# Optimization experiments

Measured on AMD Instinct MI355X. Metric: run time of the kernel, lower is better.

The kernel has to match this reference:

```python
import jax, jax.numpy as jnp
import numpy as np

# Config constants (match init_kwargs)
E = 16          # n_routed_experts
G = 4           # n_groups
TOPK_G = 2      # topk_groups
K = 4           # n_activated_experts
ROUTE_SCALE = 2.5446


def setup_inputs() -> dict:
    key = jax.random.key(0)
    ks = jax.random.split(key, 9)
    T, D, H = 2048, 1024, 704
    HS = 2 * H  # shared FFN hidden = n_shared_experts * expert_hidden_dim
    sc = lambda k, shape, fan_in: (jax.random.normal(k, shape, jnp.float32)
                                   * (fan_in ** -0.5))
    return {
        "x":      jax.random.normal(ks[0], (T, D), jnp.float32),
        "gate_w": sc(ks[1], (E, D), D),
        "gate_b": jnp.zeros((E,), jnp.float32),       # V3 routing bias (init 0)
        "w1":     sc(ks[2], (E, H, D), D),            # gate proj per expert
        "w3":     sc(ks[3], (E, H, D), D),            # up proj per expert
        "w2":     sc(ks[4], (E, D, H), H),            # down proj per expert
        "ws1":    sc(ks[5], (HS, D), D),              # shared FFN gate proj
        "ws3":    sc(ks[6], (HS, D), D),              # shared FFN up proj
        "ws2":    sc(ks[7], (D, HS), HS),             # shared FFN down proj
    }


def _gate(x, gate_w, gate_b):
    """DeepSeek-V3 sigmoid gate with bias routing + group-limited masking."""
    T = x.shape[0]
    logits = x @ gate_w.T                                   # [T, E]
    scores = jax.nn.sigmoid(logits).astype(jnp.float32)     # original_scores
    routing = scores + gate_b                               # bias only affects routing
    g = routing.reshape(T, G, E // G)
    # use_bias=True -> group score = sum of top-2 routing scores in group
    group_scores = jnp.sum(jax.lax.top_k(g, 2)[0], axis=-1)     # [T, G]
    top_groups = jax.lax.top_k(group_scores, TOPK_G)[1]         # [T, TOPK_G]
    keep = jnp.any(jnp.arange(G)[None, :, None] == top_groups[:, None, :],
                   axis=-1)                                     # [T, G]
    routing = jnp.where(keep[:, :, None], g, -jnp.inf).reshape(T, E)
    idx = jax.lax.top_k(routing, K)[1]                          # [T, K]
    w = jnp.take_along_axis(scores, idx, axis=1)                # un-biased weights
    w = w / jnp.clip(jnp.sum(w, axis=-1, keepdims=True), 1e-9)  # sigmoid renorm
    w = (w * ROUTE_SCALE).astype(x.dtype)
    return w, idx


def reference(x, gate_w, gate_b, w1, w3, w2, ws1, ws3, ws2):
    T, D = x.shape
    weights, idx = _gate(x, gate_w, gate_b)                 # [T,K], [T,K]
    # Dense dispatch/combine matrix: combine[t, e] = gate weight (0 if unrouted)
    combine = jnp.zeros((T, E), x.dtype).at[
        jnp.arange(T)[:, None], idx].add(weights)           # [T, E]
    # Routed experts: SwiGLU per expert, grouped GEMMs
    hg = jnp.einsum('td,ehd->eth', x, w1)                   # [E, T, H]
    hu = jnp.einsum('td,ehd->eth', x, w3)                   # [E, T, H]
    eo = jnp.einsum('eth,edh->etd', jax.nn.silu(hg) * hu, w2)  # [E, T, D]
    y_routed = jnp.einsum('etd,te->td', eo, combine)        # [T, D]
    # Shared experts (always active SwiGLU)
    y_shared = (jax.nn.silu(x @ ws1.T) * (x @ ws3.T)) @ ws2.T
    return y_routed + y_shared
```

## Files before the change

### kernel.cpp

```cpp
#include <hip/hip_runtime.h>
#include <hip/hip_bf16.h>
#include <math.h>

typedef __attribute__((ext_vector_type(4))) float   f32x4;
typedef __attribute__((ext_vector_type(8))) short   short8;
typedef __attribute__((ext_vector_type(8))) __bf16  bf16x8;

union SB8 { short8 s; bf16x8 b; };

__device__ __forceinline__ short f2bf(float f) {
  union { float f; unsigned u; } v; v.f = f;
  unsigned r = v.u + 0x7fffu + ((v.u >> 16) & 1u);
  return (short)(r >> 16);
}

__device__ __forceinline__ short8 cvt8(f32x4 a, f32x4 b) {
  short8 r;
  r[0] = f2bf(a[0]); r[1] = f2bf(a[1]); r[2] = f2bf(a[2]); r[3] = f2bf(a[3]);
  r[4] = f2bf(b[0]); r[5] = f2bf(b[1]); r[6] = f2bf(b[2]); r[7] = f2bf(b[3]);
  return r;
}

__device__ __forceinline__ void ldsload16(const short* g, short* l) {
  __builtin_amdgcn_global_load_lds(
      (const __attribute__((address_space(1))) unsigned int*)g,
      (__attribute__((address_space(3))) unsigned int*)l, 16, 0, 0);
}

#define TT   2048
#define DD   1024
#define HH   704
#define HSS  1408
#define EE   16
#define CAP  2048
#define CSTR 32

#define O1  2097152ULL
#define O2  13631488ULL
#define O3  25165824ULL
#define O4  36700160ULL
#define O5  38141952ULL
#define O6  39583744ULL
#define CVT_TOTAL 41025536ULL

#define W2SZ    11534336ULL
#define WS1SZ   1441792ULL
#define WS1END  26607616ULL
#define CVTA_TOTAL  28049408ULL
#define CVTA_BLOCKS 3424
#define GATE_BLOCKS 512

__global__ __launch_bounds__(256)
void gate_cvt(const float* __restrict__ x,  const float* __restrict__ w1,
              const float* __restrict__ w3, const float* __restrict__ s1,
              const float* __restrict__ s3, short* __restrict__ dst,
              const float* __restrict__ gw, const float* __restrict__ gb,
              int* __restrict__ counts, int* __restrict__ tok,
              float* __restrict__ wgt, int* __restrict__ eslot)
{
  if (blockIdx.x >= GATE_BLOCKS) {
    const int tid = threadIdx.x;
    const size_t base = (size_t)(blockIdx.x - GATE_BLOCKS) * 8192;
    const float* sp[4]; short* dp[4];
    #pragma unroll
    for (int k = 0; k < 4; k++) {
      const size_t sb = base + (size_t)k * 2048;
      const float* src; size_t doff;
      if      (sb < O1)     { src = x  + sb;            doff = sb; }
      else if (sb < O2)     { src = w1 + (sb - O1);     doff = sb; }
      else if (sb < O3)     { src = w3 + (sb - O2);     doff = sb; }
      else if (sb < WS1END) { src = s1 + (sb - O3);     doff = sb + W2SZ; }
      else                  { src = s3 + (sb - WS1END); doff = sb + W2SZ; }
      sp[k] = src + tid * 8;
      dp[k] = dst + doff + tid * 8;
    }
    f32x4 va[8];
    #pragma unroll
    for (int k = 0; k < 4; k++) {
      va[2 * k]     = *(const f32x4*)(sp[k]);
      va[2 * k + 1] = *(const f32x4*)(sp[k] + 4);
    }
    #pragma unroll
    for (int k = 0; k < 4; k++)
      *(short8*)(dp[k]) = cvt8(va[2 * k], va[2 * k + 1]);
    return;
  }

  const int lane = threadIdx.x & 63;
  const int wid  = threadIdx.x >> 6;
  const int t    = blockIdx.x * 4 + wid;
  const int e    = lane & 15;
  const int p    = lane >> 4;

  const float* xp = x + (size_t)t * DD + p * 256;
  const float* gp = gw + (size_t)e * DD + p * 256;

  double a0 = 0.0, a1 = 0.0, a2 = 0.0, a3 = 0.0;
  #pragma unroll 8
  for (int i = 0; i < 64; i++) {
    f32x4 xa = *(const f32x4*)(xp + i * 4);
    f32x4 ga = *(const f32x4*)(gp + i * 4);
    a0 += (double)xa[0] * (double)ga[0];
    a1 += (double)xa[1] * (double)ga[1];
    a2 += (double)xa[2] * (double)ga[2];
    a3 += (double)xa[3] * (double)ga[3];
  }
  double acc = (a0 + a1) + (a2 + a3);
  acc += __shfl_xor(acc, 16);
  acc += __shfl_xor(acc, 32);
  float accf = (float)acc;

  float lf[EE], sc[EE], r[EE];
  #pragma unroll
  for (int j = 0; j < EE; j++) lf[j] = __shfl(accf, j);
  #pragma unroll
  for (int j = 0; j < EE; j++) {
    sc[j] = 1.f / (1.f + expf(-lf[j]));
    r[j] = sc[j] + gb[j];
  }
  float gs[4];
  #pragma unroll
  for (int g = 0; g < 4; g++) {
    float m1 = -1e30f, m2 = -1e30f;
    #pragma unroll
    for (int j = 0; j < 4; j++) {
      float v = r[g * 4 + j];
      if (v > m1) { m2 = m1; m1 = v; }
      else if (v > m2) { m2 = v; }
    }
    gs[g] = m1 + m2;
  }
  int g1 = 0, g2 = -1; float b1 = -1e30f, b2 = -1e30f;
  #pragma unroll
  for (int g = 0; g < 4; g++) {
    if (gs[g] > b1) { b2 = b1; g2 = g1; b1 = gs[g]; g1 = g; }
    else if (gs[g] > b2) { b2 = gs[g]; g2 = g; }
  }
  int idx[4]; float wv[4]; float wsum = 0.f;
  unsigned used = 0;
  #pragma unroll
  for (int k = 0; k < 4; k++) {
    float best = -1e30f; int bi = 0;
    #pragma unroll
    for (int j = 0; j < EE; j++) {
      int g = j >> 2;
      bool keep = (g == g1) || (g == g2);
      if (keep && !((used >> j) & 1) && r[j] > best) { best = r[j]; bi = j; }
    }
    used |= 1u << bi; idx[k] = bi; wv[k] = sc[bi]; wsum += sc[bi];
  }
  float div = wsum < 1e-9f ? 1e-9f : wsum;
  if (lane < 4) {
    float w = wv[lane] / div * 2.5446f;
    int slot = atomicAdd(&counts[idx[lane] * CSTR], 1);
    tok[idx[lane] * CAP + slot] = t;
    wgt[idx[lane] * CAP + slot] = w;
    eslot[t * 4 + lane] = (idx[lane] << 16) | slot;
  }
}

#define WAIT_PREV_TILE()  do { \
    asm volatile("s_waitcnt vmcnt(4)" ::: "memory"); \
    __builtin_amdgcn_sched_barrier(0); \
    __builtin_amdgcn_s_barrier(); \
    __builtin_amdgcn_sched_barrier(0); } while (0)
#define WAIT_LAST_TILE()  do { \
    asm volatile("s_waitcnt vmcnt(0)" ::: "memory"); \
    __builtin_amdgcn_sched_barrier(0); \
    __builtin_amdgcn_s_barrier(); \
    __builtin_amdgcn_sched_barrier(0); } while (0)
#define END_TILE_BARRIER() do { \
    __builtin_amdgcn_sched_barrier(0); \
    __builtin_amdgcn_s_barrier(); } while (0)

__global__ __launch_bounds__(512, 2)
void gemm1_merged(const short* __restrict__ xb, const short* __restrict__ w1b,
                  const short* __restrict__ w3b, const short* __restrict__ ws1b,
                  const short* __restrict__ ws3b, short* __restrict__ act_r,
                  short* __restrict__ act_s, const int* __restrict__ counts,
                  const int* __restrict__ tok,
                  const float* __restrict__ w2f, const float* __restrict__ ws2f,
                  short* __restrict__ w2bd, short* __restrict__ ws2bd)
{
  const int F = blockIdx.x + 11 * (blockIdx.y + 16 * blockIdx.z);
  const int r8 = F & 7, rank = F >> 3;
  int z, Mt, Ntc;
  if (rank < 22) {
    z = 0;
    const int p = rank * 8 + r8;
    Mt = p / 11; Ntc = p - Mt * 11;
  } else if (rank < 374) {
    const int rr = rank - 22;
    z = 1 + r8 + 8 * (rr / 176);
    const int p = rr % 176;
    Mt = p / 11; Ntc = p - Mt * 11;
  } else {
    z = 17;
    const int p = (rank - 374) * 8 + r8;
    Mt = p / 22; Ntc = p - Mt * 22;
  }

  if (z == 0) {
    const int bid = Mt * 11 + Ntc;
    const int tid = threadIdx.x;
    for (int s = 0; s < 3; s++) {
      const size_t base = (size_t)bid * 73728 + (size_t)s * 24576;
      const float* sp[6]; short* dp[6];
      #pragma unroll
      for (int k = 0; k < 6; k++) {
        const size_t sb = base + (size_t)k * 4096;
        if (sb < W2SZ) {
          sp[k] = w2f + sb + tid * 8;
          dp[k] = w2bd + sb + tid * 8;
        } else {
          const size_t o = sb - W2SZ;
          sp[k] = ws2f + o + tid * 8;
          dp[k] = ws2bd + o + tid * 8;
        }
      }
      f32x4 va[12];
      #pragma unroll
      for (int k = 0; k < 6; k++) {
        va[2 * k]     = *(const f32x4*)(sp[k]);
        va[2 * k + 1] = *(const f32x4*)(sp[k] + 4);
      }
      #pragma unroll
      for (int k = 0; k < 6; k++)
        *(short8*)(dp[k]) = cvt8(va[2 * k], va[2 * k + 1]);
    }
    return;
  }

  const bool routed = (z <= EE);
  const int e = z - 1;

  int cnt, N, rowbase = 0;
  const short *W1, *W3;
  short* act;
  if (routed) {
    cnt = counts[e * CSTR];
    if (Mt * 128 >= cnt) return;
    int rb = 0;
    for (int i = 0; i < e; i++) rb += counts[i * CSTR];
    rowbase = rb;
    N = HH;
    W1 = w1b + (size_t)e * HH * DD;
    W3 = w3b + (size_t)e * HH * DD;
    act = act_r;
  } else {
    cnt = TT; N = HSS; W1 = ws1b; W3 = ws3b; act = act_s;
  }
  const int NtB = Ntc * 64;

  __shared__ __align__(16) short lA [2][128 * 64];
  __shared__ __align__(16) short lB1[2][64 * 64];
  __shared__ __align__(16) short lB3[2][64 * 64];

  const int tid = threadIdx.x, lane = tid & 63, wv = tid >> 6;
  const int srow = lane >> 3, schunk = lane & 7, scg = schunk ^ srow;

  const short* pa[2]; const short* pb1; const short* pb3;
  #pragma unroll
  for (int i = 0; i < 2; i++) {
    const int g = wv * 2 + i;
    int arow = Mt * 128 + g * 8 + srow;
    if (routed) {
      int slot = arow < cnt ? arow : cnt - 1;
      arow = tok[e * CAP + slot];
    }
    pa[i] = xb + (size_t)arow * DD + scg * 8;
  }
  {
    const int brow = NtB + wv * 8 + srow;
    pb1 = W1 + (size_t)brow * DD + scg * 8;
    pb3 = W3 + (size_t)brow * DD + scg * 8;
  }

  f32x4 acc1[4], acc3[4];
  #pragma unroll
  for (int i = 0; i < 4; i++) { acc1[i] = (f32x4)0.f; acc3[i] = (f32x4)0.f; }

  const int q = lane >> 4, r7 = lane & 7, hi = (lane & 15) >> 3;
  const int wc = wv & 3, mh = wv >> 2;

#define STAGE1(c, kk) do { \
    ldsload16(pa[0] + (kk), &lA [c][(wv * 2 + 0) * 512]); \
    ldsload16(pa[1] + (kk), &lA [c][(wv * 2 + 1) * 512]); \
    ldsload16(pb1  + (kk),  &lB1[c][wv * 512]); \
    ldsload16(pb3  + (kk),  &lB3[c][wv * 512]); } while (0)

#define GEMM1_BODY(c) do { \
    _Pragma("unroll") for (int kc = 0; kc < 2; kc++) { \
      const int cx = (kc * 4 + q) ^ r7; \
      SB8 b1f, b3f; \
      b1f.s = *(const short8*)(&lB1[c][((wc * 2 + hi) * 64 + r7 * 8 + cx) * 8]); \
      b3f.s = *(const short8*)(&lB3[c][((wc * 2 + hi) * 64 + r7 * 8 + cx) * 8]); \
      _Pragma("unroll") for (int mt = 0; mt < 4; mt++) { \
        SB8 af; af.s = *(const short8*)(&lA[c][((2 * (mh * 4 + mt) + hi) * 64 + r7 * 8 + cx) * 8]); \
        acc1[mt] = __builtin_amdgcn_mfma_f32_16x16x32_bf16(af.b, b1f.b, acc1[mt], 0, 0, 0); \
        acc3[mt] = __builtin_amdgcn_mfma_f32_16x16x32_bf16(af.b, b3f.b, acc3[mt], 0, 0, 0); \
      } } } while (0)

  STAGE1(0, 0);
  int cur = 0;
  for (int kk = 64; kk < DD; kk += 64) {
    STAGE1(cur ^ 1, kk);
    WAIT_PREV_TILE();
    GEMM1_BODY(cur);
    END_TILE_BARRIER();
    cur ^= 1;
  }
  WAIT_LAST_TILE();
  GEMM1_BODY(cur);

  const int quad = lane >> 4, lcol = lane & 15;
  const int col = NtB + wc * 16 + lcol;
  #pragma unroll
  for (int mt = 0; mt < 4; mt++) {
    #pragma unroll
    for (int rg = 0; rg < 4; rg++) {
      const int r = Mt * 128 + (mh * 4 + mt) * 16 + quad * 4 + rg;
      if (r < cnt) {
        float g = acc1[mt][rg], u = acc3[mt][rg];
        float a = g / (1.f + __expf(-g)) * u;
        act[(size_t)(rowbase + r) * N + col] = f2bf(a);
      }
    }
  }
#undef STAGE1
#undef GEMM1_BODY
}

__global__ __launch_bounds__(512, 2)
void gemm2_merged(const short* __restrict__ act_r, const short* __restrict__ act_s,
                  const short* __restrict__ w2b, const short* __restrict__ ws2b,
                  float* __restrict__ y, float* __restrict__ outr,
                  const int* __restrict__ counts, const float* __restrict__ wgt)
{
  const int F = blockIdx.x + 8 * (blockIdx.y + 16 * blockIdx.z);
  const int r8 = F & 7, rank = F >> 3;
  int z, Mt, Nt;
  if (rank < 256) {
    z = r8 + 8 * (rank >> 7);
    const int p = rank & 127;
    Mt = p >> 3; Nt = p & 7;
  } else {
    z = 16;
    const int p = (rank - 256) * 8 + r8;
    Mt = p >> 3; Nt = p & 7;
  }

  const bool routed = (z < EE);

  int cnt, Kd, rowbase = 0;
  const short *A, *W;
  if (routed) {
    cnt = counts[z * CSTR];
    if (Mt * 128 >= cnt) return;
    int rb = 0;
    for (int i = 0; i < z; i++) rb += counts[i * CSTR];
    rowbase = rb;
    Kd = HH;
    A = act_r + (size_t)rowbase * HH;
    W = w2b + (size_t)z * DD * HH;
  } else {
    cnt = TT; Kd = HSS; A = act_s; W = ws2b;
  }

  __shared__ __align__(16) short lA[2][128 * 64];
  __shared__ __align__(16) short lB[2][128 * 64];

  const int tid = threadIdx.x, lane = tid & 63, wv = tid >> 6;
  const int srow = lane >> 3, schunk = lane & 7, scg = schunk ^ srow;

  const short* pa[2]; const short* pb[2];
  #pragma unroll
  for (int i = 0; i < 2; i++) {
    const int g = wv * 2 + i;
    int arow = Mt * 128 + g * 8 + srow;
    if (arow >= cnt) arow = cnt - 1;
    pa[i] = A + (size_t)arow * Kd + scg * 8;
    const int brow = Nt * 128 + g * 8 + srow;
    pb[i] = W + (size_t)brow * Kd + scg * 8;
  }

  f32x4 acc[4][2];
  #pragma unroll
  for (int i = 0; i < 4; i++) { acc[i][0] = (f32x4)0.f; acc[i][1] = (f32x4)0.f; }

  const int q = lane >> 4, r7 = lane & 7, hi = (lane & 15) >> 3;
  const int wc = wv & 3, mh = wv >> 2;

#define STAGE2(c, kk) do { \
    ldsload16(pa[0] + (kk), &lA[c][(wv * 2 + 0) * 512]); \
    ldsload16(pa[1] + (kk), &lA[c][(wv * 2 + 1) * 512]); \
    ldsload16(pb[0] + (kk), &lB[c][(wv * 2 + 0) * 512]); \
    ldsload16(pb[1] + (kk), &lB[c][(wv * 2 + 1) * 512]); } while (0)

#define GEMM2_BODY(c) do { \
    _Pragma("unroll") for (int kc = 0; kc < 2; kc++) { \
      const int cx = (kc * 4 + q) ^ r7; \
      SB8 bf[2]; \
      _Pragma("unroll") for (int ntl = 0; ntl < 2; ntl++) { \
        const int a16 = ((wc * 2 + ntl) * 2 + hi) * 64 + r7 * 8 + cx; \
        bf[ntl].s = *(const short8*)(&lB[c][a16 * 8]); \
      } \
      _Pragma("unroll") for (int mt = 0; mt < 4; mt++) { \
        const int a16 = (2 * (mh * 4 + mt) + hi) * 64 + r7 * 8 + cx; \
        SB8 af; af.s = *(const short8*)(&lA[c][a16 * 8]); \
        acc[mt][0] = __builtin_amdgcn_mfma_f32_16x16x32_bf16(af.b, bf[0].b, acc[mt][0], 0, 0, 0); \
        acc[mt][1] = __builtin_amdgcn_mfma_f32_16x16x32_bf16(af.b, bf[1].b, acc[mt][1], 0, 0, 0); \
      } } } while (0)

  STAGE2(0, 0);
  int cur = 0;
  for (int kk = 64; kk < Kd; kk += 64) {
    STAGE2(cur ^ 1, kk);
    WAIT_PREV_TILE();
    GEMM2_BODY(cur);
    END_TILE_BARRIER();
    cur ^= 1;
  }
  WAIT_LAST_TILE();
  GEMM2_BODY(cur);

  const int quad = lane >> 4, lcol = lane & 15;
  #pragma unroll
  for (int mt = 0; mt < 4; mt++) {
    #pragma unroll
    for (int ntl = 0; ntl < 2; ntl++) {
      const int col = Nt * 128 + (wc * 2 + ntl) * 16 + lcol;
      #pragma unroll
      for (int rg = 0; rg < 4; rg++) {
        const int slot = Mt * 128 + (mh * 4 + mt) * 16 + quad * 4 + rg;
        const float v = acc[mt][ntl][rg];
        if (routed) {
          if (slot < cnt) {
            const float w = wgt[z * CAP + slot];
            outr[(size_t)(rowbase + slot) * DD + col] = w * v;
          }
        } else {
          y[(size_t)slot * DD + col] = v;
        }
      }
    }
  }
#undef STAGE2
#undef GEMM2_BODY
}

__global__ __launch_bounds__(256)
void combine_kernel(float* __restrict__ y, const float* __restrict__ outr,
                    const int* __restrict__ eslot, const int* __restrict__ counts)
{
  const int t = blockIdx.x;
  const int d = threadIdx.x * 4;

  int offs[EE];
  int s = 0;
  #pragma unroll
  for (int i = 0; i < EE; i++) { offs[i] = s; s += counts[i * CSTR]; }

  f32x4 accv = *(f32x4*)(y + (size_t)t * DD + d);
  #pragma unroll
  for (int k = 0; k < 4; k++) {
    const int es = eslot[t * 4 + k];
    const int row = offs[es >> 16] + (es & 0xFFFF);
    accv += *(const f32x4*)(outr + (size_t)row * DD + d);
  }
  *(f32x4*)(y + (size_t)t * DD + d) = accv;
}

extern "C" void kernel_launch(void* const* d_in, const int* in_sizes, int n_in,
                              void* d_out, int out_size, void* d_ws, size_t ws_size,
                              hipStream_t stream) {
  const float* x      = (const float*)d_in[0];
  const float* gate_w = (const float*)d_in[1];
  const float* gate_b = (const float*)d_in[2];
  const float* w1     = (const float*)d_in[3];
  const float* w3     = (const float*)d_in[4];
  const float* w2     = (const float*)d_in[5];
  const float* ws1    = (const float*)d_in[6];
  const float* ws3    = (const float*)d_in[7];
  const float* ws2    = (const float*)d_in[8];
  float* y = (float*)d_out;

  char* ws = (char*)d_ws;
  int*   counts = (int*)ws;
  int*   tok    = (int*)(ws + 2048);
  float* wgt    = (float*)(ws + 2048 + (size_t)EE * CAP * 4);
  int*   eslot  = (int*)(ws + 2048 + (size_t)EE * CAP * 8);
  short* bf     = (short*)(ws + 2048 + (size_t)EE * CAP * 8 + (size_t)TT * 16);
  short* xb   = bf;
  short* w1b  = bf + O1;
  short* w3b  = bf + O2;
  short* w2b  = bf + O3;
  short* ws1b = bf + O4;
  short* ws3b = bf + O5;
  short* ws2b = bf + O6;
  short* act_r = bf + CVT_TOTAL;
  short* act_s = act_r + (size_t)8192 * HH;
  float* outr = (float*)(bf + O1);

  (void)hipMemsetAsync(counts, 0, EE * CSTR * sizeof(int), stream);

  gate_cvt<<<GATE_BLOCKS + CVTA_BLOCKS, 256, 0, stream>>>(
      x, w1, w3, ws1, ws3, bf,
      gate_w, gate_b, counts, tok, wgt, eslot);

  gemm1_merged<<<dim3(11, TT / 128, EE + 3), 512, 0, stream>>>(
      xb, w1b, w3b, ws1b, ws3b, act_r, act_s, counts, tok,
      w2, ws2, w2b, ws2b);

  gemm2_merged<<<dim3(DD / 128, TT / 128, EE + 1), 512, 0, stream>>>(
      act_r, act_s, w2b, ws2b, y, outr, counts, wgt);

  combine_kernel<<<TT, 256, 0, stream>>>(y, outr, eslot, counts);
}
```

Measured before the change: 300.6 us.

## Convert weights to bf16 inside GEMM staging instead of separate pre-pass

```diff
diff --git a/kernel.cpp b/kernel.cpp
--- a/kernel.cpp
+++ b/kernel.cpp
@@ -34,26 +34,12 @@
 #define EE   16
 #define CAP  2048
 #define CSTR 32
-
-#define O1  2097152ULL
-#define O2  13631488ULL
-#define O3  25165824ULL
-#define O4  36700160ULL
-#define O5  38141952ULL
-#define O6  39583744ULL
-#define CVT_TOTAL 41025536ULL
-
-#define W2SZ    11534336ULL
-#define WS1SZ   1441792ULL
-#define WS1END  26607616ULL
-#define CVTA_TOTAL  28049408ULL
-#define CVTA_BLOCKS 3424
+#define XSZ  2097152ULL
 #define GATE_BLOCKS 512
+#define XCVT_BLOCKS 256
 
 __global__ __launch_bounds__(256)
-void gate_cvt(const float* __restrict__ x,  const float* __restrict__ w1,
-              const float* __restrict__ w3, const float* __restrict__ s1,
-              const float* __restrict__ s3, short* __restrict__ dst,
+void gate_cvt(const float* __restrict__ x, short* __restrict__ xb,
               const float* __restrict__ gw, const float* __restrict__ gb,
               int* __restrict__ counts, int* __restrict__ tok,
               float* __restrict__ wgt, int* __restrict__ eslot)
@@ -61,28 +47,15 @@
   if (blockIdx.x >= GATE_BLOCKS) {
     const int tid = threadIdx.x;
     const size_t base = (size_t)(blockIdx.x - GATE_BLOCKS) * 8192;
-    const float* sp[4]; short* dp[4];
+    f32x4 va[8];
     #pragma unroll
     for (int k = 0; k < 4; k++) {
-      const size_t sb = base + (size_t)k * 2048;
-      const float* src; size_t doff;
-      if      (sb < O1)     { src = x  + sb;            doff = sb; }
-      else if (sb < O2)     { src = w1 + (sb - O1);     doff = sb; }
-      else if (sb < O3)     { src = w3 + (sb - O2);     doff = sb; }
-      else if (sb < WS1END) { src = s1 + (sb - O3);     doff = sb + W2SZ; }
-      else                  { src = s3 + (sb - WS1END); doff = sb + W2SZ; }
-      sp[k] = src + tid * 8;
-      dp[k] = dst + doff + tid * 8;
-    }
-    f32x4 va[8];
-    #pragma unroll
-    for (int k = 0; k < 4; k++) {
-      va[2 * k]     = *(const f32x4*)(sp[k]);
-      va[2 * k + 1] = *(const f32x4*)(sp[k] + 4);
+      va[2 * k]     = *(const f32x4*)(x + base + (size_t)k * 2048 + tid * 8);
+      va[2 * k + 1] = *(const f32x4*)(x + base + (size_t)k * 2048 + tid * 8 + 4);
     }
     #pragma unroll
     for (int k = 0; k < 4; k++)
-      *(short8*)(dp[k]) = cvt8(va[2 * k], va[2 * k + 1]);
+      *(short8*)(xb + base + (size_t)k * 2048 + tid * 8) = cvt8(va[2 * k], va[2 * k + 1]);
     return;
   }
 
@@ -159,96 +132,53 @@
   }
 }
 
-#define WAIT_PREV_TILE()  do { \
-    asm volatile("s_waitcnt vmcnt(4)" ::: "memory"); \
-    __builtin_amdgcn_sched_barrier(0); \
-    __builtin_amdgcn_s_barrier(); \
-    __builtin_amdgcn_sched_barrier(0); } while (0)
-#define WAIT_LAST_TILE()  do { \
+#define PIPE_VM_WAIT() do { \
     asm volatile("s_waitcnt vmcnt(0)" ::: "memory"); \
     __builtin_amdgcn_sched_barrier(0); \
     __builtin_amdgcn_s_barrier(); \
     __builtin_amdgcn_sched_barrier(0); } while (0)
-#define END_TILE_BARRIER() do { \
+#define PIPE_LGKM_BAR() do { \
+    asm volatile("s_waitcnt lgkmcnt(0)" ::: "memory"); \
     __builtin_amdgcn_sched_barrier(0); \
-    __builtin_amdgcn_s_barrier(); } while (0)
+    __builtin_amdgcn_s_barrier(); \
+    __builtin_amdgcn_sched_barrier(0); } while (0)
 
 __global__ __launch_bounds__(512, 2)
-void gemm1_merged(const short* __restrict__ xb, const short* __restrict__ w1b,
-                  const short* __restrict__ w3b, const short* __restrict__ ws1b,
-                  const short* __restrict__ ws3b, short* __restrict__ act_r,
-                  short* __restrict__ act_s, const int* __restrict__ counts,
-                  const int* __restrict__ tok,
-                  const float* __restrict__ w2f, const float* __restrict__ ws2f,
-                  short* __restrict__ w2bd, short* __restrict__ ws2bd)
+void gemm1_merged(const short* __restrict__ xb,
+                  const float* __restrict__ w1f, const float* __restrict__ w3f,
+                  const float* __restrict__ ws1f, const float* __restrict__ ws3f,
+                  short* __restrict__ act_r, short* __restrict__ act_s,
+                  const int* __restrict__ counts, const int* __restrict__ tok)
 {
   const int F = blockIdx.x + 11 * (blockIdx.y + 16 * blockIdx.z);
   const int r8 = F & 7, rank = F >> 3;
   int z, Mt, Ntc;
-  if (rank < 22) {
-    z = 0;
-    const int p = rank * 8 + r8;
-    Mt = p / 11; Ntc = p - Mt * 11;
-  } else if (rank < 374) {
-    const int rr = rank - 22;
-    z = 1 + r8 + 8 * (rr / 176);
-    const int p = rr % 176;
-    Mt = p / 11; Ntc = p - Mt * 11;
+  if (rank < 352) {
+    z = r8 + 8 * (rank / 176);
+    const int p = rank % 176;
+    Mt = p / 11; Ntc = p % 11;
   } else {
-    z = 17;
-    const int p = (rank - 374) * 8 + r8;
-    Mt = p / 22; Ntc = p - Mt * 22;
-  }
-
-  if (z == 0) {
-    const int bid = Mt * 11 + Ntc;
-    const int tid = threadIdx.x;
-    for (int s = 0; s < 3; s++) {
-      const size_t base = (size_t)bid * 73728 + (size_t)s * 24576;
-      const float* sp[6]; short* dp[6];
-      #pragma unroll
-      for (int k = 0; k < 6; k++) {
-        const size_t sb = base + (size_t)k * 4096;
-        if (sb < W2SZ) {
-          sp[k] = w2f + sb + tid * 8;
-          dp[k] = w2bd + sb + tid * 8;
-        } else {
-          const size_t o = sb - W2SZ;
-          sp[k] = ws2f + o + tid * 8;
-          dp[k] = ws2bd + o + tid * 8;
-        }
-      }
-      f32x4 va[12];
-      #pragma unroll
-      for (int k = 0; k < 6; k++) {
-        va[2 * k]     = *(const f32x4*)(sp[k]);
-        va[2 * k + 1] = *(const f32x4*)(sp[k] + 4);
-      }
-      #pragma unroll
-      for (int k = 0; k < 6; k++)
-        *(short8*)(dp[k]) = cvt8(va[2 * k], va[2 * k + 1]);
-    }
-    return;
-  }
-
-  const bool routed = (z <= EE);
-  const int e = z - 1;
-
+    z = 16;
+    const int p = (rank - 352) * 8 + r8;
+    Mt = p / 22; Ntc = p % 22;
+  }
+
+  const bool routed = (z < EE);
   int cnt, N, rowbase = 0;
-  const short *W1, *W3;
+  const float *W1, *W3;
   short* act;
   if (routed) {
-    cnt = counts[e * CSTR];
+    cnt = counts[z * CSTR];
     if (Mt * 128 >= cnt) return;
     int rb = 0;
-    for (int i = 0; i < e; i++) rb += counts[i * CSTR];
+    for (int i = 0; i < z; i++) rb += counts[i * CSTR];
     rowbase = rb;
     N = HH;
-    W1 = w1b + (size_t)e * HH * DD;
-    W3 = w3b + (size_t)e * HH * DD;
+    W1 = w1f + (size_t)z * HH * DD;
+    W3 = w3f + (size_t)z * HH * DD;
     act = act_r;
   } else {
-    cnt = TT; N = HSS; W1 = ws1b; W3 = ws3b; act = act_s;
+    cnt = TT; N = HSS; W1 = ws1f; W3 = ws3f; act = act_s;
   }
   const int NtB = Ntc * 64;
 
@@ -259,35 +189,44 @@
   const int tid = threadIdx.x, lane = tid & 63, wv = tid >> 6;
   const int srow = lane >> 3, schunk = lane & 7, scg = schunk ^ srow;
 
-  const short* pa[2]; const short* pb1; const short* pb3;
+  const short* pa[2];
   #pragma unroll
   for (int i = 0; i < 2; i++) {
     const int g = wv * 2 + i;
     int arow = Mt * 128 + g * 8 + srow;
     if (routed) {
       int slot = arow < cnt ? arow : cnt - 1;
-      arow = tok[e * CAP + slot];
+      arow = tok[z * CAP + slot];
     }
     pa[i] = xb + (size_t)arow * DD + scg * 8;
   }
+  const float *pb1f, *pb3f;
   {
     const int brow = NtB + wv * 8 + srow;
-    pb1 = W1 + (size_t)brow * DD + scg * 8;
-    pb3 = W3 + (size_t)brow * DD + scg * 8;
+    pb1f = W1 + (size_t)brow * DD + scg * 8;
+    pb3f = W3 + (size_t)brow * DD + scg * 8;
   }
 
   f32x4 acc1[4], acc3[4];
   #pragma unroll
   for (int i = 0; i < 4; i++) { acc1[i] = (f32x4)0.f; acc3[i] = (f32x4)0.f; }
+  f32x4 rb1[2], rb3[2];
 
   const int q = lane >> 4, r7 = lane & 7, hi = (lane & 15) >> 3;
   const int wc = wv & 3, mh = wv >> 2;
-
-#define STAGE1(c, kk) do { \
-    ldsload16(pa[0] + (kk), &lA [c][(wv * 2 + 0) * 512]); \
-    ldsload16(pa[1] + (kk), &lA [c][(wv * 2 + 1) * 512]); \
-    ldsload16(pb1  + (kk),  &lB1[c][wv * 512]); \
-    ldsload16(pb3  + (kk),  &lB3[c][wv * 512]); } while (0)
+  const int wofs = wv * 512 + srow * 64 + schunk * 8;
+
+#define STAGE1_ISSUE(c, kk) do { \
+    ldsload16(pa[0] + (kk), &lA[c][(wv * 2 + 0) * 512]); \
+    ldsload16(pa[1] + (kk), &lA[c][(wv * 2 + 1) * 512]); \
+    rb1[0] = *(const f32x4*)(pb1f + (kk)); \
+    rb1[1] = *(const f32x4*)(pb1f + (kk) + 4); \
+    rb3[0] = *(const f32x4*)(pb3f + (kk)); \
+    rb3[1] = *(const f32x4*)(pb3f + (kk) + 4); } while (0)
+
+#define STAGE1_WRITE(c) do { \
+    *(short8*)(&lB1[c][wofs]) = cvt8(rb1[0], rb1[1]); \
+    *(short8*)(&lB3[c][wofs]) = cvt8(rb3[0], rb3[1]); } while (0)
 
 #define GEMM1_BODY(c) do { \
     _Pragma("unroll") for (int kc = 0; kc < 2; kc++) { \
@@ -301,16 +240,20 @@
         acc3[mt] = __builtin_amdgcn_mfma_f32_16x16x32_bf16(af.b, b3f.b, acc3[mt], 0, 0, 0); \
       } } } while (0)
 
-  STAGE1(0, 0);
+  STAGE1_ISSUE(0, 0);
+  asm volatile("s_waitcnt vmcnt(0)" ::: "memory");
+  __builtin_amdgcn_sched_barrier(0);
+  STAGE1_WRITE(0);
+  PIPE_LGKM_BAR();
   int cur = 0;
   for (int kk = 64; kk < DD; kk += 64) {
-    STAGE1(cur ^ 1, kk);
-    WAIT_PREV_TILE();
+    STAGE1_ISSUE(cur ^ 1, kk);
     GEMM1_BODY(cur);
-    END_TILE_BARRIER();
+    PIPE_VM_WAIT();
+    STAGE1_WRITE(cur ^ 1);
+    PIPE_LGKM_BAR();
     cur ^= 1;
   }
-  WAIT_LAST_TILE();
   GEMM1_BODY(cur);
 
   const int quad = lane >> 4, lcol = lane & 15;
@@ -327,13 +270,14 @@
       }
     }
   }
-#undef STAGE1
+#undef STAGE1_ISSUE
+#undef STAGE1_WRITE
 #undef GEMM1_BODY
 }
 
 __global__ __launch_bounds__(512, 2)
 void gemm2_merged(const short* __restrict__ act_r, const short* __restrict__ act_s,
-                  const short* __restrict__ w2b, const short* __restrict__ ws2b,
+                  const float* __restrict__ w2f, const float* __restrict__ ws2f,
                   float* __restrict__ y, float* __restrict__ outr,
                   const int* __restrict__ counts, const float* __restrict__ wgt)
 {
@@ -353,7 +297,8 @@
   const bool routed = (z < EE);
 
   int cnt, Kd, rowbase = 0;
-  const short *A, *W;
+  const short* A;
+  const float* W;
   if (routed) {
     cnt = counts[z * CSTR];
     if (Mt * 128 >= cnt) return;
@@ -362,9 +307,9 @@
     rowbase = rb;
     Kd = HH;
     A = act_r + (size_t)rowbase * HH;
-    W = w2b + (size_t)z * DD * HH;
+    W = w2f + (size_t)z * DD * HH;
   } else {
-    cnt = TT; Kd = HSS; A = act_s; W = ws2b;
+    cnt = TT; Kd = HSS; A = act_s; W = ws2f;
   }
 
   __shared__ __align__(16) short lA[2][128 * 64];
@@ -373,7 +318,7 @@
   const int tid = threadIdx.x, lane = tid & 63, wv = tid >> 6;
   const int srow = lane >> 3, schunk = lane & 7, scg = schunk ^ srow;
 
-  const short* pa[2]; const short* pb[2];
+  const short* pa[2]; const float* pbf[2];
   #pragma unroll
   for (int i = 0; i < 2; i++) {
     const int g = wv * 2 + i;
@@ -381,21 +326,30 @@
     if (arow >= cnt) arow = cnt - 1;
     pa[i] = A + (size_t)arow * Kd + scg * 8;
     const int brow = Nt * 128 + g * 8 + srow;
-    pb[i] = W + (size_t)brow * Kd + scg * 8;
+    pbf[i] = W + (size_t)brow * Kd + scg * 8;
   }
 
   f32x4 acc[4][2];
   #pragma unroll
   for (int i = 0; i < 4; i++) { acc[i][0] = (f32x4)0.f; acc[i][1] = (f32x4)0.f; }
+  f32x4 rbw[4];
 
   const int q = lane >> 4, r7 = lane & 7, hi = (lane & 15) >> 3;
   const int wc = wv & 3, mh = wv >> 2;
-
-#define STAGE2(c, kk) do { \
+  const int wofs0 = (wv * 2 + 0) * 512 + srow * 64 + schunk * 8;
+  const int wofs1 = (wv * 2 + 1) * 512 + srow * 64 + schunk * 8;
+
+#define STAGE2_ISSUE(c, kk) do { \
     ldsload16(pa[0] + (kk), &lA[c][(wv * 2 + 0) * 512]); \
     ldsload16(pa[1] + (kk), &lA[c][(wv * 2 + 1) * 512]); \
-    ldsload16(pb[0] + (kk), &lB[c][(wv * 2 + 0) * 512]); \
-    ldsload16(pb[1] + (kk), &lB[c][(wv * 2 + 1) * 512]); } while (0)
+    rbw[0] = *(const f32x4*)(pbf[0] + (kk)); \
+    rbw[1] = *(const f32x4*)(pbf[0] + (kk) + 4); \
+    rbw[2] = *(const f32x4*)(pbf[1] + (kk)); \
+    rbw[3] = *(const f32x4*)(pbf[1] + (kk) + 4); } while (0)
+
+#define STAGE2_WRITE(c) do { \
+    *(short8*)(&lB[c][wofs0]) = cvt8(rbw[0], rbw[1]); \
+    *(short8*)(&lB[c][wofs1]) = cvt8(rbw[2], rbw[3]); } while (0)
 
 #define GEMM2_BODY(c) do { \
     _Pragma("unroll") for (int kc = 0; kc < 2; kc++) { \
@@ -412,16 +366,20 @@
         acc[mt][1] = __builtin_amdgcn_mfma_f32_16x16x32_bf16(af.b, bf[1].b, acc[mt][1], 0, 0, 0); \
       } } } while (0)
 
-  STAGE2(0, 0);
+  STAGE2_ISSUE(0, 0);
+  asm volatile("s_waitcnt vmcnt(0)" ::: "memory");
+  __builtin_amdgcn_sched_barrier(0);
+  STAGE2_WRITE(0);
+  PIPE_LGKM_BAR();
   int cur = 0;
   for (int kk = 64; kk < Kd; kk += 64) {
-    STAGE2(cur ^ 1, kk);
-    WAIT_PREV_TILE();
+    STAGE2_ISSUE(cur ^ 1, kk);
     GEMM2_BODY(cur);
-    END_TILE_BARRIER();
+    PIPE_VM_WAIT();
+    STAGE2_WRITE(cur ^ 1);
+    PIPE_LGKM_BAR();
     cur ^= 1;
   }
-  WAIT_LAST_TILE();
   GEMM2_BODY(cur);
 
   const int quad = lane >> 4, lcol = lane & 15;
@@ -445,7 +403,8 @@
       }
     }
   }
-#undef STAGE2
+#undef STAGE2_ISSUE
+#undef STAGE2_WRITE
 #undef GEMM2_BODY
 }
 
@@ -490,30 +449,21 @@
   int*   tok    = (int*)(ws + 2048);
   float* wgt    = (float*)(ws + 2048 + (size_t)EE * CAP * 4);
   int*   eslot  = (int*)(ws + 2048 + (size_t)EE * CAP * 8);
-  short* bf     = (short*)(ws + 2048 + (size_t)EE * CAP * 8 + (size_t)TT * 16);
-  short* xb   = bf;
-  short* w1b  = bf + O1;
-  short* w3b  = bf + O2;
-  short* w2b  = bf + O3;
-  short* ws1b = bf + O4;
-  short* ws3b = bf + O5;
-  short* ws2b = bf + O6;
-  short* act_r = bf + CVT_TOTAL;
-  short* act_s = act_r + (size_t)8192 * HH;
-  float* outr = (float*)(bf + O1);
+  short* xb     = (short*)(ws + 2048 + (size_t)EE * CAP * 8 + (size_t)TT * 16);
+  short* act_r  = xb + XSZ;
+  short* act_s  = act_r + (size_t)8192 * HH;
+  float* outr   = (float*)(act_s + (size_t)TT * HSS);
 
   (void)hipMemsetAsync(counts, 0, EE * CSTR * sizeof(int), stream);
 
-  gate_cvt<<<GATE_BLOCKS + CVTA_BLOCKS, 256, 0, stream>>>(
-      x, w1, w3, ws1, ws3, bf,
-      gate_w, gate_b, counts, tok, wgt, eslot);
-
-  gemm1_merged<<<dim3(11, TT / 128, EE + 3), 512, 0, stream>>>(
-      xb, w1b, w3b, ws1b, ws3b, act_r, act_s, counts, tok,
-      w2, ws2, w2b, ws2b);
+  gate_cvt<<<GATE_BLOCKS + XCVT_BLOCKS, 256, 0, stream>>>(
+      x, xb, gate_w, gate_b, counts, tok, wgt, eslot);
+
+  gemm1_merged<<<dim3(11, TT / 128, EE + 2), 512, 0, stream>>>(
+      xb, w1, w3, ws1, ws3, act_r, act_s, counts, tok);
 
   gemm2_merged<<<dim3(DD / 128, TT / 128, EE + 1), 512, 0, stream>>>(
-      act_r, act_s, w2b, ws2b, y, outr, counts, wgt);
+      act_r, act_s, w2, ws2, y, outr, counts, wgt);
 
   combine_kernel<<<TT, 256, 0, stream>>>(y, outr, eslot, counts);
 }
```

Result: slower. 347.8 us (+15.7%).
